# Performance work log

Measured on AMD Instinct MI355X. Metric: run time of the kernel, lower is better.

Reference implementation:

```python
import jax, jax.numpy as jnp
import numpy as np

TEMPERATURE = 0.1
EPS = 1e-06


def setup_inputs() -> dict:
    key = jax.random.key(0)
    k1, k2 = jax.random.split(key)
    N, D = 8192, 256
    z1 = jax.random.normal(k1, (N, D), dtype=jnp.float32)
    z2 = jax.random.normal(k2, (N, D), dtype=jnp.float32)
    return {"z1": z1, "z2": z2}


def reference(z1, z2):
    N = z1.shape[0]
    z = jnp.concatenate([z1, z2], axis=0)                     # (2N, D)
    norm = jnp.maximum(jnp.linalg.norm(z, axis=1, keepdims=True), EPS)
    z_n = z / norm
    sim = jnp.clip(z_n @ z_n.T, -1.0 + EPS, 1.0 - EPS)        # (2N, 2N)
    diag = jnp.arange(N)
    pos_1 = sim[diag, diag + N]
    pos_2 = sim[diag + N, diag]
    positives = jnp.concatenate([pos_1, pos_2])[:, None]      # (2N, 1)
    logits = sim / TEMPERATURE
    eye = jnp.eye(2 * N, dtype=bool)
    logits_masked = jnp.where(eye, -jnp.inf, logits)
    lse = jax.nn.logsumexp(logits_masked, axis=1, keepdims=True)
    loss_per_sample = -positives / TEMPERATURE + lse
    return loss_per_sample.mean()
```

## Files before the change

### kernel.cpp

```cpp
#include <hip/hip_runtime.h>
#include <hip/hip_bf16.h>


typedef __attribute__((ext_vector_type(8)))  short  short8;
typedef __attribute__((ext_vector_type(16))) float  f32x16;
typedef __attribute__((ext_vector_type(4)))  unsigned short u16x4;

#define D 256
#define NB 64
#define TEMP_INV 10.0f

typedef __attribute__((address_space(1))) const unsigned int as1_u32;
typedef __attribute__((address_space(3))) unsigned int       as3_u32;

__device__ __forceinline__ void gload_lds16(const void* g, void* l) {
    __builtin_amdgcn_global_load_lds((as1_u32*)g, (as3_u32*)l, 16, 0, 0);
}

__device__ __forceinline__ unsigned short f2bf(float x) {
    unsigned int u = __float_as_uint(x);
    u += 0x7FFFu + ((u >> 16) & 1u);
    return (unsigned short)(u >> 16);
}

__global__ __launch_bounds__(256) void k_norm(const float* __restrict__ z1,
                                              const float* __restrict__ z2,
                                              unsigned short* __restrict__ zn,
                                              float* __restrict__ red, int N) {
    const int wv   = threadIdx.x >> 6;
    const int lane = threadIdx.x & 63;
    const int row  = blockIdx.x * 4 + wv;
    const float* src = (row < N) ? (z1 + (size_t)row * D)
                                 : (z2 + (size_t)(row - N) * D);
    float4 v = *(const float4*)(src + lane * 4);
    float s = v.x * v.x + v.y * v.y + v.z * v.z + v.w * v.w;
    #pragma unroll
    for (int off = 1; off < 64; off <<= 1) s += __shfl_xor(s, off);
    float inv = 1.0f / fmaxf(sqrtf(s), 1e-6f);
    u16x4 o;
    o.x = f2bf(v.x * inv); o.y = f2bf(v.y * inv);
    o.z = f2bf(v.z * inv); o.w = f2bf(v.w * inv);
    *(u16x4*)(zn + (size_t)row * D + lane * 4) = o;

    int tid = blockIdx.x * 256 + threadIdx.x;
    int N2 = 2 * N;
    if (tid <= N2) red[tid] = 0.0f;
}

__global__ __launch_bounds__(256, 2) void k_sim(const unsigned short* __restrict__ zn,
                                                float* __restrict__ rowsum,
                                                float* __restrict__ possum,
                                                int N2) {
    __shared__ __align__(16) char ldsB[2][16384];
    __shared__ float colsum4[4][256];

    const int tid  = threadIdx.x;
    const int lane = tid & 63;
    const int wv   = tid >> 6;
    const int l31  = lane & 31;
    const int hi   = lane >> 5;

    int p  = blockIdx.x;
    int bi = (int)((2.0f * NB + 1.0f - sqrtf((float)((2*NB+1)*(2*NB+1) - 8*p))) * 0.5f);
    while ((bi + 1) * NB - ((bi + 1) * bi) / 2 <= p) ++bi;
    while (bi * NB - (bi * (bi - 1)) / 2 > p) --bi;
    const int bj = bi + (p - (bi * NB - (bi * (bi - 1)) / 2));
    const bool diagWG = (bi == bj);
    const bool posWG  = (bj == bi + NB / 2);

    const int r0 = bi * 256 + wv * 64;

    short8 a[2][16];
    {
        const unsigned short* pA = zn + (size_t)(r0 + l31) * D + hi * 8;
        #pragma unroll
        for (int m = 0; m < 2; ++m)
            #pragma unroll
            for (int ks = 0; ks < 16; ++ks)
                a[m][ks] = *(const short8*)(pA + (size_t)m * 32 * D + ks * 16);
        #pragma unroll
        for (int m = 0; m < 2; ++m)
            #pragma unroll
            for (int ks = 0; ks < 16; ++ks)
                asm volatile("" : "+v"(a[m][ks]));
    }

    int src_off[4], lds_off[4];
    #pragma unroll
    for (int q = 0; q < 4; ++q) {
        int dl = ((q * 4 + wv) * 64 + lane) * 16;
        int row = dl >> 9;
        src_off[q] = dl ^ ((row & 31) << 4);
        lds_off[q] = (q * 4 + wv) * 1024;
    }
    const char* Bbase = (const char*)(zn + (size_t)bj * 256 * D);

#define STAGE(IT, BUF)                                                        \
    {                                                                         \
        const char* tb_ = Bbase + (IT) * 16384;                               \
        _Pragma("unroll")                                                     \
        for (int q = 0; q < 4; ++q)                                           \
            gload_lds16(tb_ + src_off[q], ldsB[BUF] + lds_off[q]);            \
    }

    float ea[2][16];
    #pragma unroll
    for (int m = 0; m < 2; ++m)
        #pragma unroll
        for (int r = 0; r < 16; ++r) ea[m][r] = 0.0f;
    float posAcc = 0.0f;

    const float SC   = 14.4269504088896341f;
    const float CLIP = 1.0f - 1e-6f;
    const int   rbase = l31 * 512;

    STAGE(0, 0);
    __syncthreads();

    for (int it = 0; it < 8; ++it) {
        const int cur = it & 1;
        if (it < 7) STAGE(it + 1, cur ^ 1);

        f32x16 acc0, acc1;
        #pragma unroll
        for (int r = 0; r < 16; ++r) { acc0[r] = 0.0f; acc1[r] = 0.0f; }

        const char* B = ldsB[cur];
        #pragma unroll
        for (int ks = 0; ks < 16; ++ks) {
            int off = rbase + ((((ks << 1) | hi) ^ l31) << 4);
            short8 b = *(const short8*)(B + off);
            acc0 = __builtin_amdgcn_mfma_f32_32x32x16_bf16(a[0][ks], b, acc0, 0, 0, 0);
            acc1 = __builtin_amdgcn_mfma_f32_32x32x16_bf16(a[1][ks], b, acc1, 0, 0, 0);
        }

        float colpart = 0.0f;
        #pragma unroll
        for (int m = 0; m < 2; ++m) {
            const bool hitTile = (it == wv * 2 + m);
            #pragma unroll
            for (int r = 0; r < 16; ++r) {
                float s = m ? acc1[r] : acc0[r];
                float e = __builtin_amdgcn_exp2f(fmaf(s, SC, -SC));
                if ((diagWG | posWG) && hitTile) {
                    int crow = (r & 3) + 8 * (r >> 2) + 4 * hi;
                    if (l31 == crow) {
                        if (diagWG) e = 0.0f;
                        else posAcc += 2.0f * fminf(fmaxf(s, -CLIP), CLIP);
                    }
                }
                ea[m][r] += e;
                colpart  += e;
            }
        }
        if (!diagWG) {
            colpart += __shfl_xor(colpart, 32);
            if (lane < 32) colsum4[wv][it * 32 + l31] = colpart;
        }
        __syncthreads();
    }

    #pragma unroll
    for (int m = 0; m < 2; ++m)
        #pragma unroll
        for (int r = 0; r < 16; ++r) {
            float v = ea[m][r];
            v += __shfl_xor(v, 1);  v += __shfl_xor(v, 2);  v += __shfl_xor(v, 4);
            v += __shfl_xor(v, 8);  v += __shfl_xor(v, 16);
            ea[m][r] = v;
        }
    if (l31 == 0) {
        #pragma unroll
        for (int m = 0; m < 2; ++m)
            #pragma unroll
            for (int r = 0; r < 16; ++r) {
                int row = r0 + m * 32 + (r & 3) + 8 * (r >> 2) + 4 * hi;
                atomicAdd(rowsum + row, ea[m][r]);
            }
    }

    if (!diagWG) {
        float cv = colsum4[0][tid] + colsum4[1][tid] + colsum4[2][tid] + colsum4[3][tid];
        atomicAdd(rowsum + bj * 256 + tid, cv);
    }

    if (posWG) {
        #pragma unroll
        for (int off = 1; off < 64; off <<= 1) posAcc += __shfl_xor(posAcc, off);
        if (lane == 0) atomicAdd(possum, posAcc);
    }
#undef STAGE
}

__global__ __launch_bounds__(1024) void k_final(const float* __restrict__ red,
                                                float* __restrict__ out, int N2) {
    __shared__ float sm[16];
    float s = 0.0f;
    for (int i = threadIdx.x; i < N2; i += 1024)
        s += __logf(red[i]);
    #pragma unroll
    for (int off = 1; off < 64; off <<= 1) s += __shfl_xor(s, off);
    const int wv = threadIdx.x >> 6, lane = threadIdx.x & 63;
    if (lane == 0) sm[wv] = s;
    __syncthreads();
    if (threadIdx.x == 0) {
        float t = 0.0f;
        #pragma unroll
        for (int w = 0; w < 16; ++w) t += sm[w];
        float possum = red[N2];
        out[0] = (t + 10.0f * (float)N2 - possum * TEMP_INV) / (float)N2;
    }
}

extern "C" void kernel_launch(void* const* d_in, const int* in_sizes, int n_in,
                              void* d_out, int out_size, void* d_ws, size_t ws_size,
                              hipStream_t stream) {
    const float* z1 = (const float*)d_in[0];
    const float* z2 = (const float*)d_in[1];
    const int N  = in_sizes[0] / D;
    const int N2 = 2 * N;

    unsigned short* zn = (unsigned short*)d_ws;
    float* red = (float*)((char*)d_ws + (size_t)N2 * D * sizeof(unsigned short));

    k_norm<<<N2 / 4, 256, 0, stream>>>(z1, z2, zn, red, N);
    k_sim<<<(NB * (NB + 1)) / 2, 256, 0, stream>>>(zn, red, red + N2, N2);
    k_final<<<1, 1024, 0, stream>>>(red, (float*)d_out, N2);
}
```

Baseline: 222.8 us.

## Use 512-thread workgroups with 32-row waves and an XCD-aware block swizzle

Each workgroup now has 8 waves. Each wave keeps 32 rows of A in registers and computes two 32-column tiles per stage against 64-column B stages (32KB of LDS per buffer), so the loop runs 4 stages instead of 8. Block IDs are remapped so consecutive triangular tiles land on the same XCD, aiming for better L2 reuse of B tiles. This lowers register pressure per wave and raises waves per workgroup, but it doubles LDS reads per MFMA pair and raises LDS use per block, which may limit how many blocks fit on a CU.

```diff
diff --git a/kernel.cpp b/kernel.cpp
--- a/kernel.cpp
+++ b/kernel.cpp
@@ -7,7 +7,6 @@
 typedef __attribute__((ext_vector_type(4)))  unsigned short u16x4;
 
 #define D 256
-#define NB 64
 #define TEMP_INV 10.0f
 
 typedef __attribute__((address_space(1))) const unsigned int as1_u32;
@@ -47,79 +46,77 @@
     if (tid <= N2) red[tid] = 0.0f;
 }
 
-__global__ __launch_bounds__(256, 2) void k_sim(const unsigned short* __restrict__ zn,
+__global__ __launch_bounds__(512, 3) void k_sim(const unsigned short* __restrict__ zn,
                                                 float* __restrict__ rowsum,
                                                 float* __restrict__ possum,
                                                 int N2) {
-    __shared__ __align__(16) char ldsB[2][16384];
-    __shared__ float colsum4[4][256];
+    __shared__ __align__(16) char ldsB[2][32768];
+    __shared__ float colsum[8][256];
 
     const int tid  = threadIdx.x;
     const int lane = tid & 63;
-    const int wv   = tid >> 6;
+    const int w    = tid >> 6;
     const int l31  = lane & 31;
     const int hi   = lane >> 5;
 
-    int p  = blockIdx.x;
-    int bi = (int)((2.0f * NB + 1.0f - sqrtf((float)((2*NB+1)*(2*NB+1) - 8*p))) * 0.5f);
-    while ((bi + 1) * NB - ((bi + 1) * bi) / 2 <= p) ++bi;
-    while (bi * NB - (bi * (bi - 1)) / 2 > p) --bi;
-    const int bj = bi + (p - (bi * NB - (bi * (bi - 1)) / 2));
+    const int NBr = N2 >> 8;
+    const int nwg = (NBr * (NBr + 1)) >> 1;
+
+    const int cpx = nwg >> 3;
+    const int bid = (int)blockIdx.x;
+    const int p   = (bid & 7) * cpx + (bid >> 3);
+
+    int bi = (int)((2.0f * NBr + 1.0f
+                    - sqrtf((float)((2 * NBr + 1) * (2 * NBr + 1) - 8 * p))) * 0.5f);
+    while ((bi + 1) * NBr - ((bi + 1) * bi) / 2 <= p) ++bi;
+    while (bi * NBr - (bi * (bi - 1)) / 2 > p) --bi;
+    const int bj = bi + (p - (bi * NBr - (bi * (bi - 1)) / 2));
     const bool diagWG = (bi == bj);
-    const bool posWG  = (bj == bi + NB / 2);
-
-    const int r0 = bi * 256 + wv * 64;
-
-    short8 a[2][16];
+    const bool posWG  = (bj == bi + (NBr >> 1));
+
+    const int r0 = bi * 256 + w * 32;
+
+    short8 a[16];
     {
         const unsigned short* pA = zn + (size_t)(r0 + l31) * D + hi * 8;
         #pragma unroll
-        for (int m = 0; m < 2; ++m)
-            #pragma unroll
-            for (int ks = 0; ks < 16; ++ks)
-                a[m][ks] = *(const short8*)(pA + (size_t)m * 32 * D + ks * 16);
-        #pragma unroll
-        for (int m = 0; m < 2; ++m)
-            #pragma unroll
-            for (int ks = 0; ks < 16; ++ks)
-                asm volatile("" : "+v"(a[m][ks]));
-    }
-
-    int src_off[4], lds_off[4];
+        for (int ks = 0; ks < 16; ++ks) a[ks] = *(const short8*)(pA + ks * 16);
+        #pragma unroll
+        for (int ks = 0; ks < 16; ++ks) asm volatile("" : "+v"(a[ks]));
+    }
+
+    int src_off[4], lds_base[4];
     #pragma unroll
     for (int q = 0; q < 4; ++q) {
-        int dl = ((q * 4 + wv) * 64 + lane) * 16;
+        int dl = ((q * 8 + w) * 64 + lane) * 16;
         int row = dl >> 9;
         src_off[q] = dl ^ ((row & 31) << 4);
-        lds_off[q] = (q * 4 + wv) * 1024;
-    }
-    const char* Bbase = (const char*)(zn + (size_t)bj * 256 * D);
+        lds_base[q] = (q * 8 + w) * 1024;
+    }
+    const char* Bbase = (const char*)zn + (size_t)bj * 256 * D * 2;
 
 #define STAGE(IT, BUF)                                                        \
     {                                                                         \
-        const char* tb_ = Bbase + (IT) * 16384;                               \
+        const char* tb_ = Bbase + (IT) * 32768;                               \
         _Pragma("unroll")                                                     \
         for (int q = 0; q < 4; ++q)                                           \
-            gload_lds16(tb_ + src_off[q], ldsB[BUF] + lds_off[q]);            \
-    }
-
-    float ea[2][16];
-    #pragma unroll
-    for (int m = 0; m < 2; ++m)
-        #pragma unroll
-        for (int r = 0; r < 16; ++r) ea[m][r] = 0.0f;
+            gload_lds16(tb_ + src_off[q], ldsB[BUF] + lds_base[q]);           \
+    }
+
+    float ea[16];
+    #pragma unroll
+    for (int r = 0; r < 16; ++r) ea[r] = 0.0f;
     float posAcc = 0.0f;
 
     const float SC   = 14.4269504088896341f;
     const float CLIP = 1.0f - 1e-6f;
-    const int   rbase = l31 * 512;
 
     STAGE(0, 0);
     __syncthreads();
 
-    for (int it = 0; it < 8; ++it) {
+    for (int it = 0; it < 4; ++it) {
         const int cur = it & 1;
-        if (it < 7) STAGE(it + 1, cur ^ 1);
+        if (it < 3) STAGE(it + 1, cur ^ 1);
 
         f32x16 acc0, acc1;
         #pragma unroll
@@ -128,59 +125,59 @@
         const char* B = ldsB[cur];
         #pragma unroll
         for (int ks = 0; ks < 16; ++ks) {
-            int off = rbase + ((((ks << 1) | hi) ^ l31) << 4);
-            short8 b = *(const short8*)(B + off);
-            acc0 = __builtin_amdgcn_mfma_f32_32x32x16_bf16(a[0][ks], b, acc0, 0, 0, 0);
-            acc1 = __builtin_amdgcn_mfma_f32_32x32x16_bf16(a[1][ks], b, acc1, 0, 0, 0);
+            int g = ((((ks << 1) | hi) ^ l31) << 4);
+            short8 b0 = *(const short8*)(B + l31 * 512 + g);
+            short8 b1 = *(const short8*)(B + (l31 + 32) * 512 + g);
+            acc0 = __builtin_amdgcn_mfma_f32_32x32x16_bf16(a[ks], b0, acc0, 0, 0, 0);
+            acc1 = __builtin_amdgcn_mfma_f32_32x32x16_bf16(a[ks], b1, acc1, 0, 0, 0);
         }
 
-        float colpart = 0.0f;
-        #pragma unroll
-        for (int m = 0; m < 2; ++m) {
-            const bool hitTile = (it == wv * 2 + m);
-            #pragma unroll
-            for (int r = 0; r < 16; ++r) {
-                float s = m ? acc1[r] : acc0[r];
-                float e = __builtin_amdgcn_exp2f(fmaf(s, SC, -SC));
-                if ((diagWG | posWG) && hitTile) {
-                    int crow = (r & 3) + 8 * (r >> 2) + 4 * hi;
-                    if (l31 == crow) {
-                        if (diagWG) e = 0.0f;
-                        else posAcc += 2.0f * fminf(fmaxf(s, -CLIP), CLIP);
+        float cp0 = 0.0f, cp1 = 0.0f;
+        const bool hitW = (diagWG | posWG) && (it == (w >> 1));
+        #pragma unroll
+        for (int r = 0; r < 16; ++r) {
+            float s0 = acc0[r], s1 = acc1[r];
+            float e0 = __builtin_amdgcn_exp2f(fmaf(s0, SC, -SC));
+            float e1 = __builtin_amdgcn_exp2f(fmaf(s1, SC, -SC));
+            if (hitW) {
+                int crow = (r & 3) + 8 * (r >> 2) + 4 * hi;
+                if (l31 == crow) {
+                    if ((w & 1) == 0) {
+                        if (diagWG) e0 = 0.0f;
+                        else posAcc += 2.0f * fminf(fmaxf(s0, -CLIP), CLIP);
+                    } else {
+                        if (diagWG) e1 = 0.0f;
+                        else posAcc += 2.0f * fminf(fmaxf(s1, -CLIP), CLIP);
                     }
                 }
-                ea[m][r] += e;
-                colpart  += e;
+            }
+            ea[r] += e0 + e1;
+            cp0 += e0;  cp1 += e1;
+        }
+        if (!diagWG) {
+            cp0 += __shfl_xor(cp0, 32);
+            cp1 += __shfl_xor(cp1, 32);
+            if (lane < 32) {
+                colsum[w][it * 64 + l31]      = cp0;
+                colsum[w][it * 64 + 32 + l31] = cp1;
             }
         }
-        if (!diagWG) {
-            colpart += __shfl_xor(colpart, 32);
-            if (lane < 32) colsum4[wv][it * 32 + l31] = colpart;
-        }
         __syncthreads();
     }
 
     #pragma unroll
-    for (int m = 0; m < 2; ++m)
-        #pragma unroll
-        for (int r = 0; r < 16; ++r) {
-            float v = ea[m][r];
-            v += __shfl_xor(v, 1);  v += __shfl_xor(v, 2);  v += __shfl_xor(v, 4);
-            v += __shfl_xor(v, 8);  v += __shfl_xor(v, 16);
-            ea[m][r] = v;
-        }
-    if (l31 == 0) {
-        #pragma unroll
-        for (int m = 0; m < 2; ++m)
-            #pragma unroll
-            for (int r = 0; r < 16; ++r) {
-                int row = r0 + m * 32 + (r & 3) + 8 * (r >> 2) + 4 * hi;
-                atomicAdd(rowsum + row, ea[m][r]);
-            }
-    }
-
-    if (!diagWG) {
-        float cv = colsum4[0][tid] + colsum4[1][tid] + colsum4[2][tid] + colsum4[3][tid];
+    for (int r = 0; r < 16; ++r) {
+        float v = ea[r];
+        v += __shfl_xor(v, 1);  v += __shfl_xor(v, 2);  v += __shfl_xor(v, 4);
+        v += __shfl_xor(v, 8);  v += __shfl_xor(v, 16);
+        if (l31 == 0)
+            atomicAdd(rowsum + r0 + (r & 3) + 8 * (r >> 2) + 4 * hi, v);
+    }
+
+    if (!diagWG && tid < 256) {
+        float cv = 0.0f;
+        #pragma unroll
+        for (int w8 = 0; w8 < 8; ++w8) cv += colsum[w8][tid];
         atomicAdd(rowsum + bj * 256 + tid, cv);
     }
 
@@ -219,11 +216,13 @@
     const float* z2 = (const float*)d_in[1];
     const int N  = in_sizes[0] / D;
     const int N2 = 2 * N;
+    const int NBr = N2 / 256;
+    const int nwg = (NBr * (NBr + 1)) / 2;
 
     unsigned short* zn = (unsigned short*)d_ws;
     float* red = (float*)((char*)d_ws + (size_t)N2 * D * sizeof(unsigned short));
 
     k_norm<<<N2 / 4, 256, 0, stream>>>(z1, z2, zn, red, N);
-    k_sim<<<(NB * (NB + 1)) / 2, 256, 0, stream>>>(zn, red, red + N2, N2);
+    k_sim<<<nwg, 512, 0, stream>>>(zn, red, red + N2, N2);
     k_final<<<1, 1024, 0, stream>>>(red, (float*)d_out, N2);
 }
```

After: 284.6 us. +27.7%, slower.
